# Kernel optimization log

Hardware: AMD Instinct MI355X
Metric: run time of the kernel (lower is better)

## Reference

```python
import jax, jax.numpy as jnp
import numpy as np

N_NODES = 50000
N_EDGES = 800000
IN_CH = 64
OUT_CH = 64
EDGE_DIM = 3


def setup_inputs() -> dict:
    key = jax.random.key(0)
    k1, k2, k3, k4, k5 = jax.random.split(key, 5)
    x = jax.random.normal(k1, (N_NODES, IN_CH), dtype=jnp.float32)
    edge_index = jax.random.randint(k2, (2, N_EDGES), 0, N_NODES, dtype=jnp.int64)
    edge_attr = jax.random.normal(k3, (N_EDGES, EDGE_DIM), dtype=jnp.float32)
    # nn.Linear default init: U(-1/sqrt(fan_in), 1/sqrt(fan_in)); weight shape [out, in]
    bound = 1.0 / np.sqrt(IN_CH)
    phi_w = jax.random.uniform(k4, (OUT_CH, IN_CH), minval=-bound, maxval=bound, dtype=jnp.float32)
    psi_w = jax.random.uniform(k5, (OUT_CH, IN_CH), minval=-bound, maxval=bound, dtype=jnp.float32)
    return {"x": x, "edge_index": edge_index, "edge_attr": edge_attr, "phi_w": phi_w, "psi_w": psi_w}


def reference(x, edge_index, edge_attr, phi_w, psi_w):
    src, dst = edge_index[0], edge_index[1]
    # gather -> linear -> scale by edge-attr L2 norm
    msg = jnp.einsum('ei,oi->eo', x[src], phi_w)  # [E, out_ch]
    msg = msg * jnp.linalg.norm(edge_attr, axis=1, keepdims=True)
    # scatter-add into destination nodes
    agg = jax.ops.segment_sum(msg, dst, num_segments=x.shape[0])  # [N, out_ch]
    return jnp.einsum('ni,oi->no', x, psi_w) + agg
```

## Files before the change

### kernel.cpp

```cpp
#include <hip/hip_runtime.h>
#include <math.h>

#define NN 50000
#define NE 800000
#define CH 64
#define CSLOT 64
#define LDA 129

typedef float v4f __attribute__((ext_vector_type(4)));

__global__ __launch_bounds__(256) void place16_k(const int* __restrict__ ei,
                                                 const float* __restrict__ ea,
                                                 int* __restrict__ count,
                                                 int4* __restrict__ slots) {
    const int e = blockIdx.x * 256 + threadIdx.x;
    if (e >= NE) return;
    const int src = ei[e];
    const int dst = ei[NE + e];
    const float a0 = ea[3 * e + 0];
    const float a1 = ea[3 * e + 1];
    const float a2 = ea[3 * e + 2];
    const float nrm = sqrtf(a0 * a0 + a1 * a1 + a2 * a2);
    const int r = atomicAdd(&count[dst], 1);
    if (r < CSLOT) {
        int4 v; v.x = src; v.y = __float_as_int(nrm); v.z = 0; v.w = 0;
        slots[(size_t)dst * CSLOT + r] = v;
    }
}

__global__ __launch_bounds__(256) void place8_k(const int* __restrict__ ei,
                                                const float* __restrict__ ea,
                                                int* __restrict__ count,
                                                int2* __restrict__ slots) {
    const int e = blockIdx.x * 256 + threadIdx.x;
    if (e >= NE) return;
    const int src = ei[e];
    const int dst = ei[NE + e];
    const float a0 = ea[3 * e + 0];
    const float a1 = ea[3 * e + 1];
    const float a2 = ea[3 * e + 2];
    const float nrm = sqrtf(a0 * a0 + a1 * a1 + a2 * a2);
    const int r = atomicAdd(&count[dst], 1);
    if (r < CSLOT) {
        int2 v; v.x = src; v.y = __float_as_int(nrm);
        slots[(size_t)dst * CSLOT + r] = v;
    }
}

__global__ __launch_bounds__(256) void agg16_k(const float* __restrict__ x,
                                               const int* __restrict__ count,
                                               const int4* __restrict__ slots,
                                               float* __restrict__ s) {
    const int c = threadIdx.x & 63;
    const int n = (int)((blockIdx.x * 256u + threadIdx.x) >> 6);
    if (n >= NN) return;
    int cnt = count[n]; if (cnt > CSLOT) cnt = CSLOT;
    const int4* sl = slots + (size_t)n * CSLOT;
    float acc0 = 0.f, acc1 = 0.f;
    int j = 0;
    for (; j + 8 <= cnt; j += 8) {
        const int4 p0 = sl[j],     p1 = sl[j + 1], p2 = sl[j + 2], p3 = sl[j + 3];
        const int4 p4 = sl[j + 4], p5 = sl[j + 5], p6 = sl[j + 6], p7 = sl[j + 7];
        const float x0 = x[(size_t)p0.x * CH + c];
        const float x1 = x[(size_t)p1.x * CH + c];
        const float x2 = x[(size_t)p2.x * CH + c];
        const float x3 = x[(size_t)p3.x * CH + c];
        const float x4 = x[(size_t)p4.x * CH + c];
        const float x5 = x[(size_t)p5.x * CH + c];
        const float x6 = x[(size_t)p6.x * CH + c];
        const float x7 = x[(size_t)p7.x * CH + c];
        acc0 = fmaf(__int_as_float(p0.y), x0, acc0);
        acc1 = fmaf(__int_as_float(p1.y), x1, acc1);
        acc0 = fmaf(__int_as_float(p2.y), x2, acc0);
        acc1 = fmaf(__int_as_float(p3.y), x3, acc1);
        acc0 = fmaf(__int_as_float(p4.y), x4, acc0);
        acc1 = fmaf(__int_as_float(p5.y), x5, acc1);
        acc0 = fmaf(__int_as_float(p6.y), x6, acc0);
        acc1 = fmaf(__int_as_float(p7.y), x7, acc1);
    }
    for (; j < cnt; ++j) {
        const int4 p = sl[j];
        acc0 = fmaf(__int_as_float(p.y), x[(size_t)p.x * CH + c], acc0);
    }
    s[(size_t)n * CH + c] = acc0 + acc1;
}

__global__ __launch_bounds__(256) void agg8_k(const float* __restrict__ x,
                                              const int* __restrict__ count,
                                              const int2* __restrict__ slots,
                                              float* __restrict__ s) {
    const int c = threadIdx.x & 63;
    const int n = (int)((blockIdx.x * 256u + threadIdx.x) >> 6);
    if (n >= NN) return;
    int cnt = count[n]; if (cnt > CSLOT) cnt = CSLOT;
    const int2* sl = slots + (size_t)n * CSLOT;
    float acc0 = 0.f, acc1 = 0.f;
    int j = 0;
    for (; j + 8 <= cnt; j += 8) {
        const int2 p0 = sl[j],     p1 = sl[j + 1], p2 = sl[j + 2], p3 = sl[j + 3];
        const int2 p4 = sl[j + 4], p5 = sl[j + 5], p6 = sl[j + 6], p7 = sl[j + 7];
        const float x0 = x[(size_t)p0.x * CH + c];
        const float x1 = x[(size_t)p1.x * CH + c];
        const float x2 = x[(size_t)p2.x * CH + c];
        const float x3 = x[(size_t)p3.x * CH + c];
        const float x4 = x[(size_t)p4.x * CH + c];
        const float x5 = x[(size_t)p5.x * CH + c];
        const float x6 = x[(size_t)p6.x * CH + c];
        const float x7 = x[(size_t)p7.x * CH + c];
        acc0 = fmaf(__int_as_float(p0.y), x0, acc0);
        acc1 = fmaf(__int_as_float(p1.y), x1, acc1);
        acc0 = fmaf(__int_as_float(p2.y), x2, acc0);
        acc1 = fmaf(__int_as_float(p3.y), x3, acc1);
        acc0 = fmaf(__int_as_float(p4.y), x4, acc0);
        acc1 = fmaf(__int_as_float(p5.y), x5, acc1);
        acc0 = fmaf(__int_as_float(p6.y), x6, acc0);
        acc1 = fmaf(__int_as_float(p7.y), x7, acc1);
    }
    for (; j < cnt; ++j) {
        const int2 p = sl[j];
        acc0 = fmaf(__int_as_float(p.y), x[(size_t)p.x * CH + c], acc0);
    }
    s[(size_t)n * CH + c] = acc0 + acc1;
}

__global__ __launch_bounds__(256) void scatter_r2(const float* __restrict__ x,
                                                  const int* __restrict__ ei,
                                                  const float* __restrict__ ea,
                                                  float* s) {
    const int lane = threadIdx.x & 63;
    int w = (int)((blockIdx.x * 256u + threadIdx.x) >> 6);
    const int nw = (int)((gridDim.x * 256u) >> 6);
    for (int e = w; e < NE; e += nw) {
        const int src = ei[e];
        const int dst = ei[NE + e];
        const float a0 = ea[3 * e + 0];
        const float a1 = ea[3 * e + 1];
        const float a2 = ea[3 * e + 2];
        const float nrm = sqrtf(a0 * a0 + a1 * a1 + a2 * a2);
        atomicAdd(&s[(size_t)dst * CH + lane], nrm * x[(size_t)src * CH + lane]);
    }
}

__global__ __launch_bounds__(256, 2) void out_gemm_k(const float* __restrict__ x,
                                                     const float* s,
                                                     const float* __restrict__ phi,
                                                     const float* __restrict__ psi,
                                                     float* out) {
    __shared__ float A[64][LDA];
    __shared__ float B[64][LDA];
    const int t = threadIdx.x;
    const int n0 = blockIdx.x * 64;

    for (int idx = t; idx < 64 * 16; idx += 256) {
        const int o = idx >> 4, j = idx & 15;
        v4f p = *(const v4f*)(psi + (size_t)o * CH + 4 * j);
        v4f q = *(const v4f*)(phi + (size_t)o * CH + 4 * j);
        *(v4f*)&B[o][4 * j] = p;
        *(v4f*)&B[o][64 + 4 * j] = q;
    }
    for (int idx = t; idx < 64 * 16; idx += 256) {
        const int r = idx >> 4, j = idx & 15;
        const int n = n0 + r;
        v4f xv = {0.f, 0.f, 0.f, 0.f}, sv = {0.f, 0.f, 0.f, 0.f};
        if (n < NN) {
            xv = *(const v4f*)(x + (size_t)n * CH + 4 * j);
            sv = *(const v4f*)(s + (size_t)n * CH + 4 * j);
        }
        *(v4f*)&A[r][4 * j] = xv;
        *(v4f*)&A[r][64 + 4 * j] = sv;
    }
    __syncthreads();

    const int r0 = (t >> 4) * 4;
    const int c0 = (t & 15) * 4;
    float acc[4][4] = {{0.f}};
#pragma clang loop unroll_count(2)
    for (int i = 0; i < 128; i += 4) {
        v4f a0 = *(const v4f*)&A[r0 + 0][i];
        v4f a1 = *(const v4f*)&A[r0 + 1][i];
        v4f a2 = *(const v4f*)&A[r0 + 2][i];
        v4f a3 = *(const v4f*)&A[r0 + 3][i];
        v4f b0 = *(const v4f*)&B[c0 + 0][i];
        v4f b1 = *(const v4f*)&B[c0 + 1][i];
        v4f b2 = *(const v4f*)&B[c0 + 2][i];
        v4f b3 = *(const v4f*)&B[c0 + 3][i];
#define FMA4(k, av)                                   \
        acc[k][0] = fmaf(av.x, b0.x, acc[k][0]);      \
        acc[k][0] = fmaf(av.y, b0.y, acc[k][0]);      \
        acc[k][0] = fmaf(av.z, b0.z, acc[k][0]);      \
        acc[k][0] = fmaf(av.w, b0.w, acc[k][0]);      \
        acc[k][1] = fmaf(av.x, b1.x, acc[k][1]);      \
        acc[k][1] = fmaf(av.y, b1.y, acc[k][1]);      \
        acc[k][1] = fmaf(av.z, b1.z, acc[k][1]);      \
        acc[k][1] = fmaf(av.w, b1.w, acc[k][1]);      \
        acc[k][2] = fmaf(av.x, b2.x, acc[k][2]);      \
        acc[k][2] = fmaf(av.y, b2.y, acc[k][2]);      \
        acc[k][2] = fmaf(av.z, b2.z, acc[k][2]);      \
        acc[k][2] = fmaf(av.w, b2.w, acc[k][2]);      \
        acc[k][3] = fmaf(av.x, b3.x, acc[k][3]);      \
        acc[k][3] = fmaf(av.y, b3.y, acc[k][3]);      \
        acc[k][3] = fmaf(av.z, b3.z, acc[k][3]);      \
        acc[k][3] = fmaf(av.w, b3.w, acc[k][3])
        FMA4(0, a0);
        FMA4(1, a1);
        FMA4(2, a2);
        FMA4(3, a3);
#undef FMA4
    }

#pragma unroll
    for (int k = 0; k < 4; ++k) {
        const int n = n0 + r0 + k;
        if (n < NN) {
            v4f v; v.x = acc[k][0]; v.y = acc[k][1]; v.z = acc[k][2]; v.w = acc[k][3];
            *(v4f*)(out + (size_t)n * CH + c0) = v;
        }
    }
}

extern "C" void kernel_launch(void* const* d_in, const int* in_sizes, int n_in,
                              void* d_out, int out_size, void* d_ws, size_t ws_size,
                              hipStream_t stream) {
    const float* x   = (const float*)d_in[0];
    const int*   ei  = (const int*)d_in[1];
    const float* ea  = (const float*)d_in[2];
    const float* phi = (const float*)d_in[3];
    const float* psi = (const float*)d_in[4];
    float* out = (float*)d_out;

    const int ngemm = (NN + 63) / 64;
    const int nedge = (NE + 255) / 256;
    const int nagg  = (NN * 64 + 255) / 256;

    const size_t need16 = (size_t)NN * CSLOT * 16 + (size_t)NN * 4;
    const size_t need8  = (size_t)NN * CSLOT * 8  + (size_t)NN * 4;

    if (ws_size >= need16) {
        int4* slots = (int4*)d_ws;
        int* count  = (int*)(slots + (size_t)NN * CSLOT);
        (void)hipMemsetAsync(count, 0, (size_t)NN * sizeof(int), stream);
        place16_k<<<nedge, 256, 0, stream>>>(ei, ea, count, slots);
        agg16_k<<<nagg, 256, 0, stream>>>(x, count, slots, out);
        out_gemm_k<<<ngemm, 256, 0, stream>>>(x, out, phi, psi, out);
    } else if (ws_size >= need8) {
        int2* slots = (int2*)d_ws;
        int* count  = (int*)(slots + (size_t)NN * CSLOT);
        (void)hipMemsetAsync(count, 0, (size_t)NN * sizeof(int), stream);
        place8_k<<<nedge, 256, 0, stream>>>(ei, ea, count, slots);
        agg8_k<<<nagg, 256, 0, stream>>>(x, count, slots, out);
        out_gemm_k<<<ngemm, 256, 0, stream>>>(x, out, phi, psi, out);
    } else {
        (void)hipMemsetAsync(out, 0, (size_t)NN * CH * sizeof(float), stream);
        scatter_r2<<<4096, 256, 0, stream>>>(x, ei, ea, out);
        out_gemm_k<<<ngemm, 256, 0, stream>>>(x, out, phi, psi, out);
    }
}
```

Before: 199.7 us.

## Gather bf16 copy of x in aggregation and partition edge placement by XCD

```diff
diff --git a/kernel.cpp b/kernel.cpp
--- a/kernel.cpp
+++ b/kernel.cpp
@@ -8,87 +8,59 @@
 #define LDA 129
 
 typedef float v4f __attribute__((ext_vector_type(4)));
-
-__global__ __launch_bounds__(256) void place16_k(const int* __restrict__ ei,
+typedef unsigned short u16x8 __attribute__((ext_vector_type(8)));
+
+__device__ __forceinline__ unsigned short f2bf(float f) {
+    unsigned int u = __float_as_uint(f);
+    unsigned int r = (u + 0x7FFFu + ((u >> 16) & 1u)) >> 16;
+    return (unsigned short)r;
+}
+__device__ __forceinline__ float bf2f(unsigned short h) {
+    return __uint_as_float(((unsigned int)h) << 16);
+}
+
+__global__ __launch_bounds__(256) void cvt_k(const float* __restrict__ x,
+                                             unsigned short* __restrict__ x16) {
+    const int i = blockIdx.x * 256 + threadIdx.x;
+    if (i * 8 >= NN * CH) return;
+    const v4f a = *(const v4f*)(x + (size_t)i * 8);
+    const v4f b = *(const v4f*)(x + (size_t)i * 8 + 4);
+    u16x8 o;
+    o[0] = f2bf(a.x); o[1] = f2bf(a.y); o[2] = f2bf(a.z); o[3] = f2bf(a.w);
+    o[4] = f2bf(b.x); o[5] = f2bf(b.y); o[6] = f2bf(b.z); o[7] = f2bf(b.w);
+    *(u16x8*)(x16 + (size_t)i * 8) = o;
+}
+
+__global__ __launch_bounds__(256) void place8x_k(const int* __restrict__ ei,
                                                  const float* __restrict__ ea,
                                                  int* __restrict__ count,
-                                                 int4* __restrict__ slots) {
-    const int e = blockIdx.x * 256 + threadIdx.x;
-    if (e >= NE) return;
-    const int src = ei[e];
-    const int dst = ei[NE + e];
-    const float a0 = ea[3 * e + 0];
-    const float a1 = ea[3 * e + 1];
-    const float a2 = ea[3 * e + 2];
-    const float nrm = sqrtf(a0 * a0 + a1 * a1 + a2 * a2);
-    const int r = atomicAdd(&count[dst], 1);
-    if (r < CSLOT) {
-        int4 v; v.x = src; v.y = __float_as_int(nrm); v.z = 0; v.w = 0;
-        slots[(size_t)dst * CSLOT + r] = v;
-    }
-}
-
-__global__ __launch_bounds__(256) void place8_k(const int* __restrict__ ei,
-                                                const float* __restrict__ ea,
-                                                int* __restrict__ count,
-                                                int2* __restrict__ slots) {
-    const int e = blockIdx.x * 256 + threadIdx.x;
-    if (e >= NE) return;
-    const int src = ei[e];
-    const int dst = ei[NE + e];
-    const float a0 = ea[3 * e + 0];
-    const float a1 = ea[3 * e + 1];
-    const float a2 = ea[3 * e + 2];
-    const float nrm = sqrtf(a0 * a0 + a1 * a1 + a2 * a2);
-    const int r = atomicAdd(&count[dst], 1);
-    if (r < CSLOT) {
-        int2 v; v.x = src; v.y = __float_as_int(nrm);
-        slots[(size_t)dst * CSLOT + r] = v;
-    }
-}
-
-__global__ __launch_bounds__(256) void agg16_k(const float* __restrict__ x,
+                                                 int2* __restrict__ slots) {
+    const int xcd  = blockIdx.x & 7;
+    const int grp  = blockIdx.x >> 3;
+    const int ngrp = gridDim.x >> 3;
+    const int per  = (NE + ngrp - 1) / ngrp;
+    const int e0 = grp * per;
+    const int e1 = (e0 + per < NE) ? e0 + per : NE;
+    for (int e = e0 + threadIdx.x; e < e1; e += 256) {
+        const int dst = ei[NE + e];
+        if ((dst & 7) != xcd) continue;
+        const int src = ei[e];
+        const float a0 = ea[3 * e + 0];
+        const float a1 = ea[3 * e + 1];
+        const float a2 = ea[3 * e + 2];
+        const float nrm = sqrtf(a0 * a0 + a1 * a1 + a2 * a2);
+        const int r = atomicAdd(&count[dst], 1);
+        if (r < CSLOT) {
+            int2 v; v.x = src; v.y = __float_as_int(nrm);
+            slots[(size_t)dst * CSLOT + r] = v;
+        }
+    }
+}
+
+__global__ __launch_bounds__(256) void agg8b_k(const unsigned short* __restrict__ x16,
                                                const int* __restrict__ count,
-                                               const int4* __restrict__ slots,
+                                               const int2* __restrict__ slots,
                                                float* __restrict__ s) {
-    const int c = threadIdx.x & 63;
-    const int n = (int)((blockIdx.x * 256u + threadIdx.x) >> 6);
-    if (n >= NN) return;
-    int cnt = count[n]; if (cnt > CSLOT) cnt = CSLOT;
-    const int4* sl = slots + (size_t)n * CSLOT;
-    float acc0 = 0.f, acc1 = 0.f;
-    int j = 0;
-    for (; j + 8 <= cnt; j += 8) {
-        const int4 p0 = sl[j],     p1 = sl[j + 1], p2 = sl[j + 2], p3 = sl[j + 3];
-        const int4 p4 = sl[j + 4], p5 = sl[j + 5], p6 = sl[j + 6], p7 = sl[j + 7];
-        const float x0 = x[(size_t)p0.x * CH + c];
-        const float x1 = x[(size_t)p1.x * CH + c];
-        const float x2 = x[(size_t)p2.x * CH + c];
-        const float x3 = x[(size_t)p3.x * CH + c];
-        const float x4 = x[(size_t)p4.x * CH + c];
-        const float x5 = x[(size_t)p5.x * CH + c];
-        const float x6 = x[(size_t)p6.x * CH + c];
-        const float x7 = x[(size_t)p7.x * CH + c];
-        acc0 = fmaf(__int_as_float(p0.y), x0, acc0);
-        acc1 = fmaf(__int_as_float(p1.y), x1, acc1);
-        acc0 = fmaf(__int_as_float(p2.y), x2, acc0);
-        acc1 = fmaf(__int_as_float(p3.y), x3, acc1);
-        acc0 = fmaf(__int_as_float(p4.y), x4, acc0);
-        acc1 = fmaf(__int_as_float(p5.y), x5, acc1);
-        acc0 = fmaf(__int_as_float(p6.y), x6, acc0);
-        acc1 = fmaf(__int_as_float(p7.y), x7, acc1);
-    }
-    for (; j < cnt; ++j) {
-        const int4 p = sl[j];
-        acc0 = fmaf(__int_as_float(p.y), x[(size_t)p.x * CH + c], acc0);
-    }
-    s[(size_t)n * CH + c] = acc0 + acc1;
-}
-
-__global__ __launch_bounds__(256) void agg8_k(const float* __restrict__ x,
-                                              const int* __restrict__ count,
-                                              const int2* __restrict__ slots,
-                                              float* __restrict__ s) {
     const int c = threadIdx.x & 63;
     const int n = (int)((blockIdx.x * 256u + threadIdx.x) >> 6);
     if (n >= NN) return;
@@ -99,14 +71,14 @@
     for (; j + 8 <= cnt; j += 8) {
         const int2 p0 = sl[j],     p1 = sl[j + 1], p2 = sl[j + 2], p3 = sl[j + 3];
         const int2 p4 = sl[j + 4], p5 = sl[j + 5], p6 = sl[j + 6], p7 = sl[j + 7];
-        const float x0 = x[(size_t)p0.x * CH + c];
-        const float x1 = x[(size_t)p1.x * CH + c];
-        const float x2 = x[(size_t)p2.x * CH + c];
-        const float x3 = x[(size_t)p3.x * CH + c];
-        const float x4 = x[(size_t)p4.x * CH + c];
-        const float x5 = x[(size_t)p5.x * CH + c];
-        const float x6 = x[(size_t)p6.x * CH + c];
-        const float x7 = x[(size_t)p7.x * CH + c];
+        const float x0 = bf2f(x16[(size_t)p0.x * CH + c]);
+        const float x1 = bf2f(x16[(size_t)p1.x * CH + c]);
+        const float x2 = bf2f(x16[(size_t)p2.x * CH + c]);
+        const float x3 = bf2f(x16[(size_t)p3.x * CH + c]);
+        const float x4 = bf2f(x16[(size_t)p4.x * CH + c]);
+        const float x5 = bf2f(x16[(size_t)p5.x * CH + c]);
+        const float x6 = bf2f(x16[(size_t)p6.x * CH + c]);
+        const float x7 = bf2f(x16[(size_t)p7.x * CH + c]);
         acc0 = fmaf(__int_as_float(p0.y), x0, acc0);
         acc1 = fmaf(__int_as_float(p1.y), x1, acc1);
         acc0 = fmaf(__int_as_float(p2.y), x2, acc0);
@@ -118,7 +90,7 @@
     }
     for (; j < cnt; ++j) {
         const int2 p = sl[j];
-        acc0 = fmaf(__int_as_float(p.y), x[(size_t)p.x * CH + c], acc0);
+        acc0 = fmaf(__int_as_float(p.y), bf2f(x16[(size_t)p.x * CH + c]), acc0);
     }
     s[(size_t)n * CH + c] = acc0 + acc1;
 }
@@ -229,25 +201,20 @@
     float* out = (float*)d_out;
 
     const int ngemm = (NN + 63) / 64;
-    const int nedge = (NE + 255) / 256;
     const int nagg  = (NN * 64 + 255) / 256;
-
-    const size_t need16 = (size_t)NN * CSLOT * 16 + (size_t)NN * 4;
-    const size_t need8  = (size_t)NN * CSLOT * 8  + (size_t)NN * 4;
-
-    if (ws_size >= need16) {
-        int4* slots = (int4*)d_ws;
-        int* count  = (int*)(slots + (size_t)NN * CSLOT);
-        (void)hipMemsetAsync(count, 0, (size_t)NN * sizeof(int), stream);
-        place16_k<<<nedge, 256, 0, stream>>>(ei, ea, count, slots);
-        agg16_k<<<nagg, 256, 0, stream>>>(x, count, slots, out);
-        out_gemm_k<<<ngemm, 256, 0, stream>>>(x, out, phi, psi, out);
-    } else if (ws_size >= need8) {
+    const int ncvt  = (NN * CH / 8 + 255) / 256;
+
+    const size_t need = (size_t)NN * CSLOT * 8 + (size_t)NN * 4 + (size_t)NN * CH * 2;
+
+    if (ws_size >= need) {
         int2* slots = (int2*)d_ws;
         int* count  = (int*)(slots + (size_t)NN * CSLOT);
+        unsigned short* x16 = (unsigned short*)(count + NN);
+
         (void)hipMemsetAsync(count, 0, (size_t)NN * sizeof(int), stream);
-        place8_k<<<nedge, 256, 0, stream>>>(ei, ea, count, slots);
-        agg8_k<<<nagg, 256, 0, stream>>>(x, count, slots, out);
+        cvt_k<<<ncvt, 256, 0, stream>>>(x, x16);
+        place8x_k<<<2048, 256, 0, stream>>>(ei, ea, count, slots);
+        agg8b_k<<<nagg, 256, 0, stream>>>(x16, count, slots, out);
         out_gemm_k<<<ngemm, 256, 0, stream>>>(x, out, phi, psi, out);
     } else {
         (void)hipMemsetAsync(out, 0, (size_t)NN * CH * sizeof(float), stream);
```

After: 186.4 us. -6.6%, faster.
